# Kernel tuning notes

Hardware: AMD Instinct MI355X
Metric: run time of the kernel (lower is better)

## Reference

```python
import jax, jax.numpy as jnp
import numpy as np

B, L, D = 4096, 50, 64
U, V, R = 100000, 100000, 5

def _lin(key, fan_out, fan_in):
    kw, kb = jax.random.split(key)
    s = 1.0 / np.sqrt(fan_in)
    return (jax.random.uniform(kw, (fan_out, fan_in), jnp.float32, -s, s),
            jax.random.uniform(kb, (fan_out,), jnp.float32, -s, s))

def setup_inputs() -> dict:
    key = jax.random.key(0)
    ks = jax.random.split(key, 12)
    w_r1_w, w_r1_b = _lin(ks[0], D, 2 * D)
    w_r2_w, w_r2_b = _lin(ks[1], D, D)
    att1_w, att1_b = _lin(ks[2], D, 2 * D)
    att2_w, att2_b = _lin(ks[3], D, D)
    att3_w, att3_b = _lin(ks[4], 1, D)
    return {
        "nodes": jax.random.randint(ks[5], (B,), 0, U),
        "history_uv": jax.random.randint(ks[6], (B, L), 0, V),
        "history_r": jax.random.randint(ks[7], (B, L), 0, R),
        "history_uvt": jax.random.randint(ks[8], (B, L), 0, 512),
        "v2e_w": jax.random.normal(ks[9], (V, D), jnp.float32) * 0.05,
        "u2e_w": jax.random.normal(ks[10], (U, D), jnp.float32) * 0.05,
        "r2e_w": jax.random.normal(ks[11], (R, D), jnp.float32) * 0.05,
        "w_r1_w": w_r1_w, "w_r1_b": w_r1_b,
        "w_r2_w": w_r2_w, "w_r2_b": w_r2_b,
        "att1_w": att1_w, "att1_b": att1_b,
        "att2_w": att2_w, "att2_b": att2_b,
        "att3_w": att3_w, "att3_b": att3_b,
    }

def reference(nodes, history_uv, history_r, history_uvt,
              v2e_w, u2e_w, r2e_w,
              w_r1_w, w_r1_b, w_r2_w, w_r2_b,
              att1_w, att1_b, att2_w, att2_b, att3_w, att3_b):
    # Gathers (uv=True branch): item embeddings for neighbor history, user rep for node
    e_uv = v2e_w[history_uv]          # (B, L, D)
    e_r = r2e_w[history_r]            # (B, L, D)
    uv_rep = u2e_w[nodes]             # (B, D)
    # Two-layer MLP on [e_uv ; e_r]
    x = jnp.concatenate([e_uv, e_r], axis=-1)               # (B, L, 2D)
    h = jax.nn.relu(jnp.einsum('blk,dk->bld', x, w_r1_w) + w_r1_b)
    o = jax.nn.relu(jnp.einsum('blk,dk->bld', h, w_r2_w) + w_r2_b)  # (B, L, D)
    # GraphRec Attention: MLP([o ; uv_rep]) -> scalar -> softmax over neighbors
    uv_b = jnp.broadcast_to(uv_rep[:, None, :], o.shape)     # (B, L, D)
    xa = jnp.concatenate([o, uv_b], axis=-1)                 # (B, L, 2D)
    a = jax.nn.relu(jnp.einsum('blk,dk->bld', xa, att1_w) + att1_b)
    a = jax.nn.relu(jnp.einsum('blk,dk->bld', a, att2_w) + att2_b)
    s = jnp.einsum('bld,od->blo', a, att3_w)[..., 0] + att3_b[0]    # (B, L)
    w = jax.nn.softmax(s, axis=1)                            # softmax over neighbors
    # att_history = o^T @ att_w  per node
    out = jnp.einsum('bld,bl->bd', o, w)                     # (B, D)
    return out
```

## Files before the change

### kernel.cpp

```cpp
#include <hip/hip_runtime.h>


#define LNB 50

typedef _Float16 f16x8 __attribute__((ext_vector_type(8)));
typedef float    f32x4 __attribute__((ext_vector_type(4)));

__device__ __forceinline__ int swz(int r, int bytecol) {
  return (r * 128 + bytecol) ^ ((r & 7) << 4);
}

__device__ __forceinline__ f16x8 cvt8(const float* __restrict__ p) {
  const float4 lo = *(const float4*)p;
  const float4 hi = *(const float4*)(p + 4);
  f16x8 a;
  a[0] = (_Float16)lo.x; a[1] = (_Float16)lo.y;
  a[2] = (_Float16)lo.z; a[3] = (_Float16)lo.w;
  a[4] = (_Float16)hi.x; a[5] = (_Float16)hi.y;
  a[6] = (_Float16)hi.z; a[7] = (_Float16)hi.w;
  return a;
}

__global__ void prep_weights(const float* __restrict__ w1, const float* __restrict__ w2,
                             const float* __restrict__ a1, const float* __restrict__ a2,
                             _Float16* __restrict__ wf) {
  int i = blockIdx.x * 256 + threadIdx.x;
  if (i < 8192) wf[i]         = (_Float16)w1[i];
  if (i < 4096) wf[8192 + i]  = (_Float16)w2[i];
  if (i < 8192) wf[12288 + i] = (_Float16)a1[i];
  if (i < 4096) wf[20480 + i] = (_Float16)a2[i];
}

__global__ __launch_bounds__(64, 2) void uvagg_fused2(
    const int* __restrict__ nodes,
    const int* __restrict__ hist_uv,
    const int* __restrict__ hist_r,
    const float* __restrict__ v2e,
    const float* __restrict__ u2e,
    const float* __restrict__ r2e,
    const float* __restrict__ b1,
    const float* __restrict__ b2,
    const float* __restrict__ ab1,
    const float* __restrict__ ab2,
    const float* __restrict__ a3w,
    const _Float16* __restrict__ wf,
    float* __restrict__ out) {
  __shared__ _Float16 T[2][64 * 64];
  __shared__ float scb[2][64];
  __shared__ float wtb[2][64];
  const int lane = threadIdx.x;
  const int lr = lane & 15;
  const int kq = lane >> 4;
  const int b0 = blockIdx.x * 2;

  const _Float16* w1f = wf;
  const _Float16* w2f = wf + 8192;
  const _Float16* a1f = wf + 12288;
  const _Float16* a2f = wf + 20480;

  {
    f16x8 Bf[4][4];
#pragma unroll
    for (int kt = 0; kt < 4; ++kt)
#pragma unroll
      for (int nt = 0; nt < 4; ++nt)
        Bf[kt][nt] = *(const f16x8*)(w1f + (nt * 16 + lr) * 128 + kt * 32 + kq * 8);

    float bias1[4];
#pragma unroll
    for (int nt = 0; nt < 4; ++nt) bias1[nt] = b1[nt * 16 + lr];

#pragma unroll
    for (int q = 0; q < 2; ++q) {
      char* Tq = (char*)T[q];
#pragma unroll
      for (int m = 0; m < 4; ++m) {
        const int rr = (b0 + q) * LNB + (m * 16 + lr < LNB ? m * 16 + lr : LNB - 1);
        const int iu = hist_uv[rr];
        const int ir = hist_r[rr];
        const float* pu = v2e + (size_t)iu * 64;
        const float* pr = r2e + (size_t)ir * 64;
        f16x8 A[4];
        A[0] = cvt8(pu + kq * 8);
        A[1] = cvt8(pu + 32 + kq * 8);
        A[2] = cvt8(pr + kq * 8);
        A[3] = cvt8(pr + 32 + kq * 8);
#pragma unroll
        for (int nt = 0; nt < 4; ++nt) {
          f32x4 acc = {0.f, 0.f, 0.f, 0.f};
#pragma unroll
          for (int kt = 0; kt < 4; ++kt)
            acc = __builtin_amdgcn_mfma_f32_16x16x32_f16(A[kt], Bf[kt][nt], acc, 0, 0, 0);
          const int c = nt * 16 + lr;
#pragma unroll
          for (int j = 0; j < 4; ++j) {
            const int row = m * 16 + kq * 4 + j;
            const float v = fmaxf(acc[j] + bias1[nt], 0.f);
            *(_Float16*)(Tq + swz(row, 2 * c)) = (_Float16)v;
          }
        }
      }
    }
  }
  __syncthreads();

  f16x8 HA0[2][4], HA1[2][4];
#pragma unroll
  for (int q = 0; q < 2; ++q) {
    const char* Tq = (const char*)T[q];
#pragma unroll
    for (int m = 0; m < 4; ++m) {
      const int r = m * 16 + lr;
      HA0[q][m] = *(const f16x8*)(Tq + swz(r, 2 * (kq * 8)));
      HA1[q][m] = *(const f16x8*)(Tq + swz(r, 2 * (32 + kq * 8)));
    }
  }
  __syncthreads();

  {
    f16x8 Bf[2][4];
#pragma unroll
    for (int kt = 0; kt < 2; ++kt)
#pragma unroll
      for (int nt = 0; nt < 4; ++nt)
        Bf[kt][nt] = *(const f16x8*)(w2f + (nt * 16 + lr) * 64 + kt * 32 + kq * 8);

    float bias2[4];
#pragma unroll
    for (int nt = 0; nt < 4; ++nt) bias2[nt] = b2[nt * 16 + lr];

#pragma unroll
    for (int q = 0; q < 2; ++q) {
      char* Tq = (char*)T[q];
#pragma unroll
      for (int m = 0; m < 4; ++m) {
#pragma unroll
        for (int nt = 0; nt < 4; ++nt) {
          f32x4 acc = {0.f, 0.f, 0.f, 0.f};
          acc = __builtin_amdgcn_mfma_f32_16x16x32_f16(HA0[q][m], Bf[0][nt], acc, 0, 0, 0);
          acc = __builtin_amdgcn_mfma_f32_16x16x32_f16(HA1[q][m], Bf[1][nt], acc, 0, 0, 0);
          const int c = nt * 16 + lr;
#pragma unroll
          for (int j = 0; j < 4; ++j) {
            const int row = m * 16 + kq * 4 + j;
            const float v = fmaxf(acc[j] + bias2[nt], 0.f);
            *(_Float16*)(Tq + swz(row, 2 * c)) = (_Float16)v;
          }
        }
      }
    }
  }
  __syncthreads();

  f16x8 OA0[2][4], OA1[2][4];
#pragma unroll
  for (int q = 0; q < 2; ++q) {
    const char* Tq = (const char*)T[q];
#pragma unroll
    for (int m = 0; m < 4; ++m) {
      const int r = m * 16 + lr;
      OA0[q][m] = *(const f16x8*)(Tq + swz(r, 2 * (kq * 8)));
      OA1[q][m] = *(const f16x8*)(Tq + swz(r, 2 * (32 + kq * 8)));
    }
  }
  __syncthreads();

  {
    f32x4 acc_u[2][4];
    {
      f16x8 Bu[2][4];
#pragma unroll
      for (int kt = 0; kt < 2; ++kt)
#pragma unroll
        for (int nt = 0; nt < 4; ++nt)
          Bu[kt][nt] = *(const f16x8*)(a1f + (nt * 16 + lr) * 128 + (kt + 2) * 32 + kq * 8);
#pragma unroll
      for (int q = 0; q < 2; ++q) {
        const int node = nodes[b0 + q];
        const f16x8 U2 = cvt8(u2e + (size_t)node * 64 + kq * 8);
        const f16x8 U3 = cvt8(u2e + (size_t)node * 64 + 32 + kq * 8);
#pragma unroll
        for (int nt = 0; nt < 4; ++nt) {
          f32x4 acc = {0.f, 0.f, 0.f, 0.f};
          acc = __builtin_amdgcn_mfma_f32_16x16x32_f16(U2, Bu[0][nt], acc, 0, 0, 0);
          acc = __builtin_amdgcn_mfma_f32_16x16x32_f16(U3, Bu[1][nt], acc, 0, 0, 0);
          acc_u[q][nt] = acc;
        }
      }
    }

    f16x8 Bf[2][4];
#pragma unroll
    for (int kt = 0; kt < 2; ++kt)
#pragma unroll
      for (int nt = 0; nt < 4; ++nt)
        Bf[kt][nt] = *(const f16x8*)(a1f + (nt * 16 + lr) * 128 + kt * 32 + kq * 8);

    float biasa1[4];
#pragma unroll
    for (int nt = 0; nt < 4; ++nt) biasa1[nt] = ab1[nt * 16 + lr];

#pragma unroll
    for (int q = 0; q < 2; ++q) {
      char* Tq = (char*)T[q];
#pragma unroll
      for (int m = 0; m < 4; ++m) {
#pragma unroll
        for (int nt = 0; nt < 4; ++nt) {
          f32x4 acc = acc_u[q][nt];
          acc = __builtin_amdgcn_mfma_f32_16x16x32_f16(OA0[q][m], Bf[0][nt], acc, 0, 0, 0);
          acc = __builtin_amdgcn_mfma_f32_16x16x32_f16(OA1[q][m], Bf[1][nt], acc, 0, 0, 0);
          const int c = nt * 16 + lr;
#pragma unroll
          for (int j = 0; j < 4; ++j) {
            const int row = m * 16 + kq * 4 + j;
            const float v = fmaxf(acc[j] + biasa1[nt], 0.f);
            *(_Float16*)(Tq + swz(row, 2 * c)) = (_Float16)v;
          }
        }
      }
    }
  }
  __syncthreads();

  {
    f16x8 Bf[2][4];
#pragma unroll
    for (int kt = 0; kt < 2; ++kt)
#pragma unroll
      for (int nt = 0; nt < 4; ++nt)
        Bf[kt][nt] = *(const f16x8*)(a2f + (nt * 16 + lr) * 64 + kt * 32 + kq * 8);

    float biasa2[4], a3c[4];
#pragma unroll
    for (int nt = 0; nt < 4; ++nt) {
      biasa2[nt] = ab2[nt * 16 + lr];
      a3c[nt] = a3w[nt * 16 + lr];
    }

#pragma unroll
    for (int m = 0; m < 4; ++m) {
      const int r = m * 16 + lr;
      f16x8 A0q[2], A1q[2];
#pragma unroll
      for (int q = 0; q < 2; ++q) {
        const char* Tq = (const char*)T[q];
        A0q[q] = *(const f16x8*)(Tq + swz(r, 2 * (kq * 8)));
        A1q[q] = *(const f16x8*)(Tq + swz(r, 2 * (32 + kq * 8)));
      }
      float part[2][4] = {{0.f,0.f,0.f,0.f},{0.f,0.f,0.f,0.f}};
#pragma unroll
      for (int nt = 0; nt < 4; ++nt) {
#pragma unroll
        for (int q = 0; q < 2; ++q) {
          f32x4 acc = {0.f, 0.f, 0.f, 0.f};
          acc = __builtin_amdgcn_mfma_f32_16x16x32_f16(A0q[q], Bf[0][nt], acc, 0, 0, 0);
          acc = __builtin_amdgcn_mfma_f32_16x16x32_f16(A1q[q], Bf[1][nt], acc, 0, 0, 0);
#pragma unroll
          for (int j = 0; j < 4; ++j) {
            const float v = fmaxf(acc[j] + biasa2[nt], 0.f);
            part[q][j] += v * a3c[nt];
          }
        }
      }
#pragma unroll
      for (int mask = 1; mask < 16; mask <<= 1)
#pragma unroll
        for (int q = 0; q < 2; ++q)
#pragma unroll
          for (int j = 0; j < 4; ++j) part[q][j] += __shfl_xor(part[q][j], mask);
      if (lr == 0) {
#pragma unroll
        for (int q = 0; q < 2; ++q)
#pragma unroll
          for (int j = 0; j < 4; ++j) scb[q][m * 16 + kq * 4 + j] = part[q][j];
      }
    }
  }
  __syncthreads();

  {
    float sv[2], mx[2], e[2], s[2];
#pragma unroll
    for (int q = 0; q < 2; ++q) { sv[q] = (lane < LNB) ? scb[q][lane] : -1e30f; mx[q] = sv[q]; }
#pragma unroll
    for (int mask = 1; mask < 64; mask <<= 1)
#pragma unroll
      for (int q = 0; q < 2; ++q) mx[q] = fmaxf(mx[q], __shfl_xor(mx[q], mask));
#pragma unroll
    for (int q = 0; q < 2; ++q) { e[q] = __expf(sv[q] - mx[q]); s[q] = e[q]; }
#pragma unroll
    for (int mask = 1; mask < 64; mask <<= 1)
#pragma unroll
      for (int q = 0; q < 2; ++q) s[q] += __shfl_xor(s[q], mask);
#pragma unroll
    for (int q = 0; q < 2; ++q) wtb[q][lane] = (lane < LNB) ? (e[q] / s[q]) : 0.f;
  }
  __syncthreads();

  {
    float wrow[2][4];
#pragma unroll
    for (int q = 0; q < 2; ++q)
#pragma unroll
      for (int m = 0; m < 4; ++m) wrow[q][m] = wtb[q][m * 16 + lr];

    float p0[2][8] = {{0,0,0,0,0,0,0,0},{0,0,0,0,0,0,0,0}};
    float p1[2][8] = {{0,0,0,0,0,0,0,0},{0,0,0,0,0,0,0,0}};
#pragma unroll
    for (int q = 0; q < 2; ++q)
#pragma unroll
      for (int m = 0; m < 4; ++m)
#pragma unroll
        for (int i = 0; i < 8; ++i) {
          p0[q][i] += wrow[q][m] * (float)OA0[q][m][i];
          p1[q][i] += wrow[q][m] * (float)OA1[q][m][i];
        }
#pragma unroll
    for (int mask = 1; mask < 16; mask <<= 1)
#pragma unroll
      for (int q = 0; q < 2; ++q)
#pragma unroll
        for (int i = 0; i < 8; ++i) {
          p0[q][i] += __shfl_xor(p0[q][i], mask);
          p1[q][i] += __shfl_xor(p1[q][i], mask);
        }
    if (lr == 0) {
#pragma unroll
      for (int q = 0; q < 2; ++q)
#pragma unroll
        for (int i = 0; i < 8; ++i) {
          scb[q][kq * 8 + i] = p0[q][i];
          scb[q][32 + kq * 8 + i] = p1[q][i];
        }
    }
  }
  __syncthreads();
#pragma unroll
  for (int q = 0; q < 2; ++q)
    out[(size_t)(b0 + q) * 64 + lane] = scb[q][lane];
}

extern "C" void kernel_launch(void* const* d_in, const int* in_sizes, int n_in,
                              void* d_out, int out_size, void* d_ws, size_t ws_size,
                              hipStream_t stream) {
  (void)in_sizes; (void)n_in; (void)out_size; (void)ws_size;
  const int* nodes = (const int*)d_in[0];
  const int* huv   = (const int*)d_in[1];
  const int* hr    = (const int*)d_in[2];
  const float* v2e = (const float*)d_in[4];
  const float* u2e = (const float*)d_in[5];
  const float* r2e = (const float*)d_in[6];
  const float* w1  = (const float*)d_in[7];
  const float* b1  = (const float*)d_in[8];
  const float* w2  = (const float*)d_in[9];
  const float* b2  = (const float*)d_in[10];
  const float* a1  = (const float*)d_in[11];
  const float* ab1 = (const float*)d_in[12];
  const float* a2  = (const float*)d_in[13];
  const float* ab2 = (const float*)d_in[14];
  const float* a3  = (const float*)d_in[15];

  _Float16* wf = (_Float16*)d_ws;
  prep_weights<<<32, 256, 0, stream>>>(w1, w2, a1, a2, wf);
  uvagg_fused2<<<2048, 64, 0, stream>>>(nodes, huv, hr, v2e, u2e, r2e,
                                        b1, b2, ab1, ab2, a3, wf,
                                        (float*)d_out);
}
```

Baseline: 144.8 us.

## Split fused kernel into dense MLP kernel and attention kernel via fp16 workspace

```diff
diff --git a/kernel.cpp b/kernel.cpp
--- a/kernel.cpp
+++ b/kernel.cpp
@@ -31,19 +31,125 @@
   if (i < 4096) wf[20480 + i] = (_Float16)a2[i];
 }
 
-__global__ __launch_bounds__(64, 2) void uvagg_fused2(
-    const int* __restrict__ nodes,
+__global__ __launch_bounds__(64, 2) void mlp_kernel(
     const int* __restrict__ hist_uv,
     const int* __restrict__ hist_r,
     const float* __restrict__ v2e,
-    const float* __restrict__ u2e,
     const float* __restrict__ r2e,
     const float* __restrict__ b1,
     const float* __restrict__ b2,
+    const _Float16* __restrict__ wf,
+    _Float16* __restrict__ ows) {
+  __shared__ _Float16 T[64 * 64];
+  const int lane = threadIdx.x;
+  const int lr = lane & 15;
+  const int kq = lane >> 4;
+  const int r0 = blockIdx.x * 64;
+
+  const _Float16* w1f = wf;
+  const _Float16* w2f = wf + 8192;
+
+  {
+    f16x8 Bf[4][4];
+#pragma unroll
+    for (int kt = 0; kt < 4; ++kt)
+#pragma unroll
+      for (int nt = 0; nt < 4; ++nt)
+        Bf[kt][nt] = *(const f16x8*)(w1f + (nt * 16 + lr) * 128 + kt * 32 + kq * 8);
+
+    float bias1[4];
+#pragma unroll
+    for (int nt = 0; nt < 4; ++nt) bias1[nt] = b1[nt * 16 + lr];
+
+#pragma unroll
+    for (int m = 0; m < 4; ++m) {
+      const int r = r0 + m * 16 + lr;
+      const int iu = hist_uv[r];
+      const int ir = hist_r[r];
+      const float* pu = v2e + (size_t)iu * 64;
+      const float* pr = r2e + (size_t)ir * 64;
+      f16x8 A[4];
+      A[0] = cvt8(pu + kq * 8);
+      A[1] = cvt8(pu + 32 + kq * 8);
+      A[2] = cvt8(pr + kq * 8);
+      A[3] = cvt8(pr + 32 + kq * 8);
+#pragma unroll
+      for (int nt = 0; nt < 4; ++nt) {
+        f32x4 acc = {0.f, 0.f, 0.f, 0.f};
+#pragma unroll
+        for (int kt = 0; kt < 4; ++kt)
+          acc = __builtin_amdgcn_mfma_f32_16x16x32_f16(A[kt], Bf[kt][nt], acc, 0, 0, 0);
+        const int c = nt * 16 + lr;
+#pragma unroll
+        for (int j = 0; j < 4; ++j) {
+          const int row = m * 16 + kq * 4 + j;
+          const float v = fmaxf(acc[j] + bias1[nt], 0.f);
+          *(_Float16*)((char*)T + swz(row, 2 * c)) = (_Float16)v;
+        }
+      }
+    }
+  }
+  __syncthreads();
+
+  f16x8 HA0[4], HA1[4];
+#pragma unroll
+  for (int m = 0; m < 4; ++m) {
+    const int r = m * 16 + lr;
+    HA0[m] = *(const f16x8*)((char*)T + swz(r, 2 * (kq * 8)));
+    HA1[m] = *(const f16x8*)((char*)T + swz(r, 2 * (32 + kq * 8)));
+  }
+  __syncthreads();
+
+  {
+    f16x8 Bf[2][4];
+#pragma unroll
+    for (int kt = 0; kt < 2; ++kt)
+#pragma unroll
+      for (int nt = 0; nt < 4; ++nt)
+        Bf[kt][nt] = *(const f16x8*)(w2f + (nt * 16 + lr) * 64 + kt * 32 + kq * 8);
+
+    float bias2[4];
+#pragma unroll
+    for (int nt = 0; nt < 4; ++nt) bias2[nt] = b2[nt * 16 + lr];
+
+#pragma unroll
+    for (int m = 0; m < 4; ++m) {
+#pragma unroll
+      for (int nt = 0; nt < 4; ++nt) {
+        f32x4 acc = {0.f, 0.f, 0.f, 0.f};
+        acc = __builtin_amdgcn_mfma_f32_16x16x32_f16(HA0[m], Bf[0][nt], acc, 0, 0, 0);
+        acc = __builtin_amdgcn_mfma_f32_16x16x32_f16(HA1[m], Bf[1][nt], acc, 0, 0, 0);
+        const int c = nt * 16 + lr;
+#pragma unroll
+        for (int j = 0; j < 4; ++j) {
+          const int row = m * 16 + kq * 4 + j;
+          const float v = fmaxf(acc[j] + bias2[nt], 0.f);
+          *(_Float16*)((char*)T + swz(row, 2 * c)) = (_Float16)v;
+        }
+      }
+    }
+  }
+  __syncthreads();
+
+  {
+    char* dst = (char*)ows + (size_t)r0 * 128;
+#pragma unroll
+    for (int p = 0; p < 8; ++p) {
+      const int idx = p * 1024 + lane * 16;
+      f16x8 v = *(const f16x8*)((const char*)T + swz(idx >> 7, idx & 127));
+      *(f16x8*)(dst + idx) = v;
+    }
+  }
+}
+
+__global__ __launch_bounds__(64, 2) void att2_kernel(
+    const int* __restrict__ nodes,
+    const float* __restrict__ u2e,
     const float* __restrict__ ab1,
     const float* __restrict__ ab2,
     const float* __restrict__ a3w,
     const _Float16* __restrict__ wf,
+    const _Float16* __restrict__ ows,
     float* __restrict__ out) {
   __shared__ _Float16 T[2][64 * 64];
   __shared__ float scb[2][64];
@@ -53,117 +159,25 @@
   const int kq = lane >> 4;
   const int b0 = blockIdx.x * 2;
 
-  const _Float16* w1f = wf;
-  const _Float16* w2f = wf + 8192;
   const _Float16* a1f = wf + 12288;
   const _Float16* a2f = wf + 20480;
 
-  {
-    f16x8 Bf[4][4];
-#pragma unroll
-    for (int kt = 0; kt < 4; ++kt)
-#pragma unroll
-      for (int nt = 0; nt < 4; ++nt)
-        Bf[kt][nt] = *(const f16x8*)(w1f + (nt * 16 + lr) * 128 + kt * 32 + kq * 8);
-
-    float bias1[4];
-#pragma unroll
-    for (int nt = 0; nt < 4; ++nt) bias1[nt] = b1[nt * 16 + lr];
-
-#pragma unroll
-    for (int q = 0; q < 2; ++q) {
-      char* Tq = (char*)T[q];
-#pragma unroll
-      for (int m = 0; m < 4; ++m) {
-        const int rr = (b0 + q) * LNB + (m * 16 + lr < LNB ? m * 16 + lr : LNB - 1);
-        const int iu = hist_uv[rr];
-        const int ir = hist_r[rr];
-        const float* pu = v2e + (size_t)iu * 64;
-        const float* pr = r2e + (size_t)ir * 64;
-        f16x8 A[4];
-        A[0] = cvt8(pu + kq * 8);
-        A[1] = cvt8(pu + 32 + kq * 8);
-        A[2] = cvt8(pr + kq * 8);
-        A[3] = cvt8(pr + 32 + kq * 8);
-#pragma unroll
-        for (int nt = 0; nt < 4; ++nt) {
-          f32x4 acc = {0.f, 0.f, 0.f, 0.f};
-#pragma unroll
-          for (int kt = 0; kt < 4; ++kt)
-            acc = __builtin_amdgcn_mfma_f32_16x16x32_f16(A[kt], Bf[kt][nt], acc, 0, 0, 0);
-          const int c = nt * 16 + lr;
-#pragma unroll
-          for (int j = 0; j < 4; ++j) {
-            const int row = m * 16 + kq * 4 + j;
-            const float v = fmaxf(acc[j] + bias1[nt], 0.f);
-            *(_Float16*)(Tq + swz(row, 2 * c)) = (_Float16)v;
-          }
-        }
-      }
-    }
-  }
-  __syncthreads();
-
-  f16x8 HA0[2][4], HA1[2][4];
+  f16x8 OA0[2][4], OA1[2][4];
 #pragma unroll
   for (int q = 0; q < 2; ++q) {
-    const char* Tq = (const char*)T[q];
+    const _Float16* ob = ows + (size_t)(b0 + q) * LNB * 64;
 #pragma unroll
     for (int m = 0; m < 4; ++m) {
       const int r = m * 16 + lr;
-      HA0[q][m] = *(const f16x8*)(Tq + swz(r, 2 * (kq * 8)));
-      HA1[q][m] = *(const f16x8*)(Tq + swz(r, 2 * (32 + kq * 8)));
-    }
-  }
-  __syncthreads();
-
-  {
-    f16x8 Bf[2][4];
-#pragma unroll
-    for (int kt = 0; kt < 2; ++kt)
-#pragma unroll
-      for (int nt = 0; nt < 4; ++nt)
-        Bf[kt][nt] = *(const f16x8*)(w2f + (nt * 16 + lr) * 64 + kt * 32 + kq * 8);
-
-    float bias2[4];
-#pragma unroll
-    for (int nt = 0; nt < 4; ++nt) bias2[nt] = b2[nt * 16 + lr];
-
-#pragma unroll
-    for (int q = 0; q < 2; ++q) {
-      char* Tq = (char*)T[q];
-#pragma unroll
-      for (int m = 0; m < 4; ++m) {
-#pragma unroll
-        for (int nt = 0; nt < 4; ++nt) {
-          f32x4 acc = {0.f, 0.f, 0.f, 0.f};
-          acc = __builtin_amdgcn_mfma_f32_16x16x32_f16(HA0[q][m], Bf[0][nt], acc, 0, 0, 0);
-          acc = __builtin_amdgcn_mfma_f32_16x16x32_f16(HA1[q][m], Bf[1][nt], acc, 0, 0, 0);
-          const int c = nt * 16 + lr;
-#pragma unroll
-          for (int j = 0; j < 4; ++j) {
-            const int row = m * 16 + kq * 4 + j;
-            const float v = fmaxf(acc[j] + bias2[nt], 0.f);
-            *(_Float16*)(Tq + swz(row, 2 * c)) = (_Float16)v;
-          }
-        }
-      }
-    }
-  }
-  __syncthreads();
-
-  f16x8 OA0[2][4], OA1[2][4];
-#pragma unroll
-  for (int q = 0; q < 2; ++q) {
-    const char* Tq = (const char*)T[q];
-#pragma unroll
-    for (int m = 0; m < 4; ++m) {
-      const int r = m * 16 + lr;
-      OA0[q][m] = *(const f16x8*)(Tq + swz(r, 2 * (kq * 8)));
-      OA1[q][m] = *(const f16x8*)(Tq + swz(r, 2 * (32 + kq * 8)));
-    }
-  }
-  __syncthreads();
+      if (r < LNB) {
+        OA0[q][m] = *(const f16x8*)(ob + (size_t)r * 64 + kq * 8);
+        OA1[q][m] = *(const f16x8*)(ob + (size_t)r * 64 + 32 + kq * 8);
+      } else {
+#pragma unroll
+        for (int i = 0; i < 8; ++i) { OA0[q][m][i] = (_Float16)0.f; OA1[q][m][i] = (_Float16)0.f; }
+      }
+    }
+  }
 
   {
     f32x4 acc_u[2][4];
@@ -361,9 +375,11 @@
   const float* ab2 = (const float*)d_in[14];
   const float* a3  = (const float*)d_in[15];
 
-  _Float16* wf = (_Float16*)d_ws;
+  _Float16* wf  = (_Float16*)d_ws;
+  _Float16* ows = (_Float16*)((char*)d_ws + 65536);
+
   prep_weights<<<32, 256, 0, stream>>>(w1, w2, a1, a2, wf);
-  uvagg_fused2<<<2048, 64, 0, stream>>>(nodes, huv, hr, v2e, u2e, r2e,
-                                        b1, b2, ab1, ab2, a3, wf,
-                                        (float*)d_out);
-}
+  mlp_kernel<<<3200, 64, 0, stream>>>(huv, hr, v2e, r2e, b1, b2, wf, ows);
+  att2_kernel<<<2048, 64, 0, stream>>>(nodes, u2e, ab1, ab2, a3, wf, ows,
+                                       (float*)d_out);
+}
```

After: 160.0 us. 1.11x slower.
